# Optimization experiments

Hardware: AMD Instinct MI355X
Metric: run time of the kernel (lower is better)

## Reference

```python
import jax, jax.numpy as jnp
import numpy as np

# --- configuration (matches init_kwargs) ---
K = 8            # number of cluster fields
L = 8            # hashgrid levels
T = 2 ** 18      # hash table size per level (log2_hashmap_size=18)
F = 2            # features per level
HID = 64         # MLP hidden dim
BASE_RES = 16    # base resolution; max_res=2048 -> growth factor 2
N_PTS = 524288

PRIMES = np.array([1, 2654435761, 805459861], dtype=np.uint32)
RES = (BASE_RES * 2 ** np.arange(L)).astype(np.float32)  # [16,32,...,2048]
CORNERS = np.array([[i, j, k] for i in (0, 1) for j in (0, 1) for k in (0, 1)],
                   dtype=np.float32)  # [8,3] trilinear corner offsets


def setup_inputs() -> dict:
    key = jax.random.key(0)
    ks = jax.random.split(key, 6)
    return {
        "positions": jax.random.uniform(ks[0], (N_PTS, 3), dtype=jnp.float32),
        "centroids": jax.random.uniform(ks[1], (K, 3), dtype=jnp.float32),
        "tables":    jax.random.normal(ks[2], (K, L, T, F), dtype=jnp.float32) * 1e-2,
        "W1":        jax.random.normal(ks[3], (K, L * F, HID), dtype=jnp.float32) * 0.1,
        "b1":        jnp.zeros((K, HID), dtype=jnp.float32),
        "W2":        jax.random.normal(ks[4], (K, HID, 1), dtype=jnp.float32) * 0.1,
        "b2":        jnp.zeros((K, 1), dtype=jnp.float32),
    }


def _hash_encode(positions, tables, assign):
    """Multi-resolution hash encoding, table selected per-point by cluster assignment."""
    N = positions.shape[0]
    res = jnp.asarray(RES)                                    # [L]
    scaled = positions[:, None, :] * res[None, :, None]       # [N,L,3]
    f = jnp.floor(scaled)
    w = scaled - f                                            # [N,L,3] trilinear fracs
    corners = jnp.asarray(CORNERS)                            # [8,3]
    ci = (f[:, :, None, :] + corners[None, None]).astype(jnp.uint32)  # [N,L,8,3]
    p = jnp.asarray(PRIMES)
    h = (ci[..., 0] * p[0]) ^ (ci[..., 1] * p[1]) ^ (ci[..., 2] * p[2])
    h = (h & jnp.uint32(T - 1)).astype(jnp.int32)             # [N,L,8]
    lvl = jnp.arange(L, dtype=jnp.int32)
    # flat index into [K*L*T, F] table selects the assigned field's grid
    flat = (assign[:, None, None] * L + lvl[None, :, None]) * T + h   # [N,L,8]
    feats = tables.reshape(K * L * T, F)[flat]                # [N,L,8,F] gather
    cw = jnp.prod(jnp.where(corners[None, None] > 0.5,
                            w[:, :, None, :], 1.0 - w[:, :, None, :]), axis=-1)  # [N,L,8]
    enc = jnp.sum(feats * cw[..., None], axis=2)              # [N,L,F]
    return enc.reshape(N, L * F)


def reference(positions, centroids, tables, W1, b1, W2, b2):
    # cdist + argmin cluster routing
    d2 = jnp.sum((positions[:, None, :] - centroids[None]) ** 2, axis=-1)  # [N,K]
    assign = jnp.argmin(d2, axis=1).astype(jnp.int32)                      # [N]
    enc = _hash_encode(positions, tables, assign)                          # [N, L*F]
    dens = jnp.zeros((positions.shape[0], 1), dtype=positions.dtype)
    for k in range(K):  # small fixed loop over structurally distinct fields
        h = jax.nn.relu(enc @ W1[k] + b1[k])
        dk = jnp.exp(h @ W2[k] + b2[k])  # trunc_exp density activation
        dens = jnp.where((assign == k)[:, None], dk, dens)
    return dens  # [N,1]
```

## Files before the change

kernel.cpp:

```cpp
#include <hip/hip_runtime.h>
#include <hip/hip_fp16.h>
#include <math.h>

#define KF 8
#define LL 8
#define TT (1 << 18)
#define FF 2
#define HID 64
#define INF 16
#define W1S 1056
#define BS  68

#define NENT (KF * LL * TT)


__global__ __launch_bounds__(256) void repack_tables_fp16(
    const float4* __restrict__ src, uint4* __restrict__ dst, int nthreads)
{
    const int gid = blockIdx.x * blockDim.x + threadIdx.x;
    if (gid >= nthreads) return;
    const size_t b = (size_t)gid * 4;

    const float4 f0 = src[b + 0];
    const float4 f1 = src[b + 1];
    const float4 f2 = src[b + 2];
    const float4 f3 = src[b + 3];

    uint4 d0, d1;
    {
        __half2 h;
        h = __floats2half2_rn(f0.x, f0.y); d0.x = *reinterpret_cast<unsigned*>(&h);
        h = __floats2half2_rn(f0.z, f0.w); d0.y = *reinterpret_cast<unsigned*>(&h);
        h = __floats2half2_rn(f1.x, f1.y); d0.z = *reinterpret_cast<unsigned*>(&h);
        h = __floats2half2_rn(f1.z, f1.w); d0.w = *reinterpret_cast<unsigned*>(&h);
        h = __floats2half2_rn(f2.x, f2.y); d1.x = *reinterpret_cast<unsigned*>(&h);
        h = __floats2half2_rn(f2.z, f2.w); d1.y = *reinterpret_cast<unsigned*>(&h);
        h = __floats2half2_rn(f3.x, f3.y); d1.z = *reinterpret_cast<unsigned*>(&h);
        h = __floats2half2_rn(f3.z, f3.w); d1.w = *reinterpret_cast<unsigned*>(&h);
    }
    dst[(size_t)gid * 2 + 0] = d0;
    dst[(size_t)gid * 2 + 1] = d1;
}

__global__ __launch_bounds__(256) void propnet_density_kernel_h(
    const float* __restrict__ positions,
    const float* __restrict__ centroids,
    const __half2* __restrict__ tables,
    const float* __restrict__ W1,
    const float* __restrict__ b1,
    const float* __restrict__ W2,
    const float* __restrict__ b2,
    float* __restrict__ out,
    int npts)
{
    __shared__ float sW1[KF * W1S];
    __shared__ float sB1[KF * BS];
    __shared__ float sW2[KF * BS];
    __shared__ float sB2[KF];
    __shared__ float sC[KF * 3];

    const int tid = threadIdx.x;

    for (int idx = tid; idx < KF * INF * HID; idx += blockDim.x) {
        int k = idx >> 10;
        int r = idx & 1023;
        sW1[k * W1S + r] = W1[idx];
    }
    for (int idx = tid; idx < KF * HID; idx += blockDim.x) {
        int k = idx >> 6;
        int r = idx & 63;
        sB1[k * BS + r] = b1[idx];
        sW2[k * BS + r] = W2[idx];
    }
    if (tid < KF) sB2[tid] = b2[tid];
    if (tid < KF * 3) sC[tid] = centroids[tid];
    __syncthreads();

    const int gid = blockIdx.x * blockDim.x + tid;
    if (gid >= npts) return;

    const float px = positions[gid * 3 + 0];
    const float py = positions[gid * 3 + 1];
    const float pz = positions[gid * 3 + 2];

    int assign = 0;
    float best = 1e30f;
    #pragma unroll
    for (int k = 0; k < KF; ++k) {
        float dx = px - sC[k * 3 + 0];
        float dy = py - sC[k * 3 + 1];
        float dz = pz - sC[k * 3 + 2];
        float d2 = fmaf(dx, dx, fmaf(dy, dy, dz * dz));
        bool lt = d2 < best;
        assign = lt ? k : assign;
        best = lt ? d2 : best;
    }

    float enc[INF];
    const __half2* __restrict__ tab =
        tables + (size_t)assign * (LL * (size_t)TT);

    #pragma unroll
    for (int l = 0; l < LL; ++l) {
        const float res = (float)(16 << l);
        const float sx = px * res, sy = py * res, sz = pz * res;
        const float fx = floorf(sx), fy = floorf(sy), fz = floorf(sz);
        const float wx = sx - fx, wy = sy - fy, wz = sz - fz;
        const unsigned ix = (unsigned)(int)fx;
        const unsigned iy = (unsigned)(int)fy;
        const unsigned iz = (unsigned)(int)fz;

        const __half2* __restrict__ tl = tab + (size_t)l * TT;

        const unsigned hx0 = ix;
        const unsigned hx1 = ix + 1u;
        const unsigned hy0 = iy * 2654435761u;
        const unsigned hy1 = (iy + 1u) * 2654435761u;
        const unsigned hz0 = iz * 805459861u;
        const unsigned hz1 = (iz + 1u) * 805459861u;
        const unsigned M = TT - 1;

        const __half2 c000 = tl[(hx0 ^ hy0 ^ hz0) & M];
        const __half2 c001 = tl[(hx0 ^ hy0 ^ hz1) & M];
        const __half2 c010 = tl[(hx0 ^ hy1 ^ hz0) & M];
        const __half2 c011 = tl[(hx0 ^ hy1 ^ hz1) & M];
        const __half2 c100 = tl[(hx1 ^ hy0 ^ hz0) & M];
        const __half2 c101 = tl[(hx1 ^ hy0 ^ hz1) & M];
        const __half2 c110 = tl[(hx1 ^ hy1 ^ hz0) & M];
        const __half2 c111 = tl[(hx1 ^ hy1 ^ hz1) & M];

        const float ux = 1.f - wx, uy = 1.f - wy, uz = 1.f - wz;
        const float w000 = ux * uy * uz, w001 = ux * uy * wz;
        const float w010 = ux * wy * uz, w011 = ux * wy * wz;
        const float w100 = wx * uy * uz, w101 = wx * uy * wz;
        const float w110 = wx * wy * uz, w111 = wx * wy * wz;

        enc[l * 2 + 0] = __low2float(c000) * w000 + __low2float(c001) * w001
                       + __low2float(c010) * w010 + __low2float(c011) * w011
                       + __low2float(c100) * w100 + __low2float(c101) * w101
                       + __low2float(c110) * w110 + __low2float(c111) * w111;
        enc[l * 2 + 1] = __high2float(c000) * w000 + __high2float(c001) * w001
                       + __high2float(c010) * w010 + __high2float(c011) * w011
                       + __high2float(c100) * w100 + __high2float(c101) * w101
                       + __high2float(c110) * w110 + __high2float(c111) * w111;
    }

    const float4* __restrict__ w1k = (const float4*)(sW1 + assign * W1S);
    const float4* __restrict__ b1k = (const float4*)(sB1 + assign * BS);
    const float4* __restrict__ w2k = (const float4*)(sW2 + assign * BS);

    float outv = sB2[assign];
    #pragma unroll
    for (int j4 = 0; j4 < HID / 4; ++j4) {
        float4 a = b1k[j4];
        #pragma unroll
        for (int i = 0; i < INF; ++i) {
            const float4 w = w1k[i * (HID / 4) + j4];
            const float e = enc[i];
            a.x = fmaf(e, w.x, a.x);
            a.y = fmaf(e, w.y, a.y);
            a.z = fmaf(e, w.z, a.z);
            a.w = fmaf(e, w.w, a.w);
        }
        a.x = fmaxf(a.x, 0.f); a.y = fmaxf(a.y, 0.f);
        a.z = fmaxf(a.z, 0.f); a.w = fmaxf(a.w, 0.f);
        const float4 w2v = w2k[j4];
        outv = fmaf(a.x, w2v.x, outv);
        outv = fmaf(a.y, w2v.y, outv);
        outv = fmaf(a.z, w2v.z, outv);
        outv = fmaf(a.w, w2v.w, outv);
    }

    out[gid] = expf(outv);
}

__global__ __launch_bounds__(256) void propnet_density_kernel_f(
    const float* __restrict__ positions,
    const float* __restrict__ centroids,
    const float* __restrict__ tables,
    const float* __restrict__ W1,
    const float* __restrict__ b1,
    const float* __restrict__ W2,
    const float* __restrict__ b2,
    float* __restrict__ out,
    int npts)
{
    __shared__ float sW1[KF * W1S];
    __shared__ float sB1[KF * BS];
    __shared__ float sW2[KF * BS];
    __shared__ float sB2[KF];
    __shared__ float sC[KF * 3];

    const int tid = threadIdx.x;

    for (int idx = tid; idx < KF * INF * HID; idx += blockDim.x) {
        int k = idx >> 10;
        int r = idx & 1023;
        sW1[k * W1S + r] = W1[idx];
    }
    for (int idx = tid; idx < KF * HID; idx += blockDim.x) {
        int k = idx >> 6;
        int r = idx & 63;
        sB1[k * BS + r] = b1[idx];
        sW2[k * BS + r] = W2[idx];
    }
    if (tid < KF) sB2[tid] = b2[tid];
    if (tid < KF * 3) sC[tid] = centroids[tid];
    __syncthreads();

    const int gid = blockIdx.x * blockDim.x + tid;
    if (gid >= npts) return;

    const float px = positions[gid * 3 + 0];
    const float py = positions[gid * 3 + 1];
    const float pz = positions[gid * 3 + 2];

    int assign = 0;
    float best = 1e30f;
    #pragma unroll
    for (int k = 0; k < KF; ++k) {
        float dx = px - sC[k * 3 + 0];
        float dy = py - sC[k * 3 + 1];
        float dz = pz - sC[k * 3 + 2];
        float d2 = fmaf(dx, dx, fmaf(dy, dy, dz * dz));
        bool lt = d2 < best;
        assign = lt ? k : assign;
        best = lt ? d2 : best;
    }

    float enc[INF];
    const float2* __restrict__ tab =
        (const float2*)tables + (size_t)assign * (LL * (size_t)TT);

    #pragma unroll
    for (int l = 0; l < LL; ++l) {
        const float res = (float)(16 << l);
        const float sx = px * res, sy = py * res, sz = pz * res;
        const float fx = floorf(sx), fy = floorf(sy), fz = floorf(sz);
        const float wx = sx - fx, wy = sy - fy, wz = sz - fz;
        const unsigned ix = (unsigned)(int)fx;
        const unsigned iy = (unsigned)(int)fy;
        const unsigned iz = (unsigned)(int)fz;

        const float2* __restrict__ tl = tab + (size_t)l * TT;

        const unsigned hx0 = ix;
        const unsigned hx1 = ix + 1u;
        const unsigned hy0 = iy * 2654435761u;
        const unsigned hy1 = (iy + 1u) * 2654435761u;
        const unsigned hz0 = iz * 805459861u;
        const unsigned hz1 = (iz + 1u) * 805459861u;
        const unsigned M = TT - 1;

        const float2 c000 = tl[(hx0 ^ hy0 ^ hz0) & M];
        const float2 c001 = tl[(hx0 ^ hy0 ^ hz1) & M];
        const float2 c010 = tl[(hx0 ^ hy1 ^ hz0) & M];
        const float2 c011 = tl[(hx0 ^ hy1 ^ hz1) & M];
        const float2 c100 = tl[(hx1 ^ hy0 ^ hz0) & M];
        const float2 c101 = tl[(hx1 ^ hy0 ^ hz1) & M];
        const float2 c110 = tl[(hx1 ^ hy1 ^ hz0) & M];
        const float2 c111 = tl[(hx1 ^ hy1 ^ hz1) & M];

        const float ux = 1.f - wx, uy = 1.f - wy, uz = 1.f - wz;
        const float w000 = ux * uy * uz, w001 = ux * uy * wz;
        const float w010 = ux * wy * uz, w011 = ux * wy * wz;
        const float w100 = wx * uy * uz, w101 = wx * uy * wz;
        const float w110 = wx * wy * uz, w111 = wx * wy * wz;

        enc[l * 2 + 0] = c000.x * w000 + c001.x * w001 + c010.x * w010 + c011.x * w011
                       + c100.x * w100 + c101.x * w101 + c110.x * w110 + c111.x * w111;
        enc[l * 2 + 1] = c000.y * w000 + c001.y * w001 + c010.y * w010 + c011.y * w011
                       + c100.y * w100 + c101.y * w101 + c110.y * w110 + c111.y * w111;
    }

    const float4* __restrict__ w1k = (const float4*)(sW1 + assign * W1S);
    const float4* __restrict__ b1k = (const float4*)(sB1 + assign * BS);
    const float4* __restrict__ w2k = (const float4*)(sW2 + assign * BS);

    float outv = sB2[assign];
    #pragma unroll
    for (int j4 = 0; j4 < HID / 4; ++j4) {
        float4 a = b1k[j4];
        #pragma unroll
        for (int i = 0; i < INF; ++i) {
            const float4 w = w1k[i * (HID / 4) + j4];
            const float e = enc[i];
            a.x = fmaf(e, w.x, a.x);
            a.y = fmaf(e, w.y, a.y);
            a.z = fmaf(e, w.z, a.z);
            a.w = fmaf(e, w.w, a.w);
        }
        a.x = fmaxf(a.x, 0.f); a.y = fmaxf(a.y, 0.f);
        a.z = fmaxf(a.z, 0.f); a.w = fmaxf(a.w, 0.f);
        const float4 w2v = w2k[j4];
        outv = fmaf(a.x, w2v.x, outv);
        outv = fmaf(a.y, w2v.y, outv);
        outv = fmaf(a.z, w2v.z, outv);
        outv = fmaf(a.w, w2v.w, outv);
    }

    out[gid] = expf(outv);
}

extern "C" void kernel_launch(void* const* d_in, const int* in_sizes, int n_in,
                              void* d_out, int out_size, void* d_ws, size_t ws_size,
                              hipStream_t stream) {
    const float* positions = (const float*)d_in[0];
    const float* centroids = (const float*)d_in[1];
    const float* tables    = (const float*)d_in[2];
    const float* W1        = (const float*)d_in[3];
    const float* b1        = (const float*)d_in[4];
    const float* W2        = (const float*)d_in[5];
    const float* b2        = (const float*)d_in[6];
    float* out = (float*)d_out;

    const int npts = in_sizes[0] / 3;
    const int block = 256;
    const int grid = (npts + block - 1) / block;

    const size_t needed = (size_t)NENT * sizeof(__half2);
    if (ws_size >= needed && d_ws != nullptr) {
        const int nthreads = NENT / 8;
        const int rgrid = nthreads / 256;
        repack_tables_fp16<<<rgrid, 256, 0, stream>>>(
            (const float4*)tables, (uint4*)d_ws, nthreads);
        propnet_density_kernel_h<<<grid, block, 0, stream>>>(
            positions, centroids, (const __half2*)d_ws, W1, b1, W2, b2, out, npts);
    } else {
        propnet_density_kernel_f<<<grid, block, 0, stream>>>(
            positions, centroids, tables, W1, b1, W2, b2, out, npts);
    }
}
```

Baseline: 415.6 us.

## Bucket points by cluster before encoding so blocks run a single field

Adds a bucketing pass that computes each point's cluster assignment and scatters point indices into per-cluster lists using block-local and global atomic counters. The main kernel then launches 8x blocks, one cluster per block, so each block loads only that cluster's MLP weights into shared memory and all threads gather from one table. The aim is to cut shared-memory footprint (raising occupancy) and improve table locality. In exchange it adds two extra launches and an index buffer, makes position reads and output writes indirect (scattered), and launches many blocks that exit immediately.

Result: slower. 438.4 us (+5.5%).

```diff
diff --git a/kernel.cpp b/kernel.cpp
--- a/kernel.cpp
+++ b/kernel.cpp
@@ -12,6 +12,7 @@
 #define BS  68
 
 #define NENT (KF * LL * TT)
+#define TAB_BYTES ((size_t)NENT * 4)
 
 
 __global__ __launch_bounds__(256) void repack_tables_fp16(
@@ -42,63 +43,95 @@
     dst[(size_t)gid * 2 + 1] = d1;
 }
 
-__global__ __launch_bounds__(256) void propnet_density_kernel_h(
+__global__ void zero_cursors(unsigned* __restrict__ cursors)
+{
+    if (threadIdx.x < KF) cursors[threadIdx.x] = 0u;
+}
+
+__global__ __launch_bounds__(256) void bucket_points(
     const float* __restrict__ positions,
     const float* __restrict__ centroids,
+    unsigned* __restrict__ cursors,
+    unsigned* __restrict__ indices,
+    int npts)
+{
+    __shared__ float sC[KF * 3];
+    __shared__ unsigned lcnt[KF];
+    __shared__ unsigned lbase[KF];
+
+    const int tid = threadIdx.x;
+    if (tid < KF * 3) sC[tid] = centroids[tid];
+    if (tid < KF) lcnt[tid] = 0u;
+    __syncthreads();
+
+    const int gid = blockIdx.x * blockDim.x + tid;
+    int assign = 0;
+    unsigned lrank = 0;
+    const bool valid = (gid < npts);
+    if (valid) {
+        const float px = positions[gid * 3 + 0];
+        const float py = positions[gid * 3 + 1];
+        const float pz = positions[gid * 3 + 2];
+        float best = 1e30f;
+        #pragma unroll
+        for (int k = 0; k < KF; ++k) {
+            float dx = px - sC[k * 3 + 0];
+            float dy = py - sC[k * 3 + 1];
+            float dz = pz - sC[k * 3 + 2];
+            float d2 = fmaf(dx, dx, fmaf(dy, dy, dz * dz));
+            bool lt = d2 < best;
+            assign = lt ? k : assign;
+            best = lt ? d2 : best;
+        }
+        lrank = atomicAdd(&lcnt[assign], 1u);
+    }
+    __syncthreads();
+    if (tid < KF) lbase[tid] = atomicAdd(&cursors[tid], lcnt[tid]);
+    __syncthreads();
+    if (valid)
+        indices[(size_t)assign * npts + lbase[assign] + lrank] = (unsigned)gid;
+}
+
+__global__ __launch_bounds__(256) void propnet_density_bucketed(
+    const float* __restrict__ positions,
     const __half2* __restrict__ tables,
     const float* __restrict__ W1,
     const float* __restrict__ b1,
     const float* __restrict__ W2,
     const float* __restrict__ b2,
+    const unsigned* __restrict__ cursors,
+    const unsigned* __restrict__ indices,
     float* __restrict__ out,
     int npts)
 {
-    __shared__ float sW1[KF * W1S];
-    __shared__ float sB1[KF * BS];
-    __shared__ float sW2[KF * BS];
-    __shared__ float sB2[KF];
-    __shared__ float sC[KF * 3];
+    const int k = blockIdx.x & 7;
+    const int s = blockIdx.x >> 3;
+    const unsigned nk = cursors[k];
+    if ((unsigned)(s * 256) >= nk) return;
+
+    __shared__ float sW1[INF * HID];
+    __shared__ float sB1[HID];
+    __shared__ float sW2[HID];
 
     const int tid = threadIdx.x;
-
-    for (int idx = tid; idx < KF * INF * HID; idx += blockDim.x) {
-        int k = idx >> 10;
-        int r = idx & 1023;
-        sW1[k * W1S + r] = W1[idx];
-    }
-    for (int idx = tid; idx < KF * HID; idx += blockDim.x) {
-        int k = idx >> 6;
-        int r = idx & 63;
-        sB1[k * BS + r] = b1[idx];
-        sW2[k * BS + r] = W2[idx];
-    }
-    if (tid < KF) sB2[tid] = b2[tid];
-    if (tid < KF * 3) sC[tid] = centroids[tid];
+    for (int idx = tid; idx < INF * HID; idx += blockDim.x)
+        sW1[idx] = W1[k * (INF * HID) + idx];
+    if (tid < HID) {
+        sB1[tid] = b1[k * HID + tid];
+        sW2[tid] = W2[k * HID + tid];
+    }
     __syncthreads();
 
-    const int gid = blockIdx.x * blockDim.x + tid;
-    if (gid >= npts) return;
-
-    const float px = positions[gid * 3 + 0];
-    const float py = positions[gid * 3 + 1];
-    const float pz = positions[gid * 3 + 2];
-
-    int assign = 0;
-    float best = 1e30f;
-    #pragma unroll
-    for (int k = 0; k < KF; ++k) {
-        float dx = px - sC[k * 3 + 0];
-        float dy = py - sC[k * 3 + 1];
-        float dz = pz - sC[k * 3 + 2];
-        float d2 = fmaf(dx, dx, fmaf(dy, dy, dz * dz));
-        bool lt = d2 < best;
-        assign = lt ? k : assign;
-        best = lt ? d2 : best;
-    }
+    const unsigned pos_in_bucket = (unsigned)(s * 256 + tid);
+    if (pos_in_bucket >= nk) return;
+    const unsigned pidx = indices[(size_t)k * npts + pos_in_bucket];
+
+    const float px = positions[pidx * 3 + 0];
+    const float py = positions[pidx * 3 + 1];
+    const float pz = positions[pidx * 3 + 2];
 
     float enc[INF];
-    const __half2* __restrict__ tab =
-        tables + (size_t)assign * (LL * (size_t)TT);
+    const __half2* __restrict__ tab = tables + (size_t)k * (LL * (size_t)TT);
 
     #pragma unroll
     for (int l = 0; l < LL; ++l) {
@@ -145,11 +178,11 @@
                        + __high2float(c110) * w110 + __high2float(c111) * w111;
     }
 
-    const float4* __restrict__ w1k = (const float4*)(sW1 + assign * W1S);
-    const float4* __restrict__ b1k = (const float4*)(sB1 + assign * BS);
-    const float4* __restrict__ w2k = (const float4*)(sW2 + assign * BS);
-
-    float outv = sB2[assign];
+    const float4* __restrict__ w1k = (const float4*)sW1;
+    const float4* __restrict__ b1k = (const float4*)sB1;
+    const float4* __restrict__ w2k = (const float4*)sW2;
+
+    float outv = b2[k];
     #pragma unroll
     for (int j4 = 0; j4 < HID / 4; ++j4) {
         float4 a = b1k[j4];
@@ -171,13 +204,13 @@
         outv = fmaf(a.w, w2v.w, outv);
     }
 
-    out[gid] = expf(outv);
-}
-
-__global__ __launch_bounds__(256) void propnet_density_kernel_f(
+    out[pidx] = expf(outv);
+}
+
+__global__ __launch_bounds__(256) void propnet_density_kernel_h(
     const float* __restrict__ positions,
     const float* __restrict__ centroids,
-    const float* __restrict__ tables,
+    const __half2* __restrict__ tables,
     const float* __restrict__ W1,
     const float* __restrict__ b1,
     const float* __restrict__ W2,
@@ -229,8 +262,8 @@
     }
 
     float enc[INF];
-    const float2* __restrict__ tab =
-        (const float2*)tables + (size_t)assign * (LL * (size_t)TT);
+    const __half2* __restrict__ tab =
+        tables + (size_t)assign * (LL * (size_t)TT);
 
     #pragma unroll
     for (int l = 0; l < LL; ++l) {
@@ -242,7 +275,7 @@
         const unsigned iy = (unsigned)(int)fy;
         const unsigned iz = (unsigned)(int)fz;
 
-        const float2* __restrict__ tl = tab + (size_t)l * TT;
+        const __half2* __restrict__ tl = tab + (size_t)l * TT;
 
         const unsigned hx0 = ix;
         const unsigned hx1 = ix + 1u;
@@ -252,14 +285,14 @@
         const unsigned hz1 = (iz + 1u) * 805459861u;
         const unsigned M = TT - 1;
 
-        const float2 c000 = tl[(hx0 ^ hy0 ^ hz0) & M];
-        const float2 c001 = tl[(hx0 ^ hy0 ^ hz1) & M];
-        const float2 c010 = tl[(hx0 ^ hy1 ^ hz0) & M];
-        const float2 c011 = tl[(hx0 ^ hy1 ^ hz1) & M];
-        const float2 c100 = tl[(hx1 ^ hy0 ^ hz0) & M];
-        const float2 c101 = tl[(hx1 ^ hy0 ^ hz1) & M];
-        const float2 c110 = tl[(hx1 ^ hy1 ^ hz0) & M];
-        const float2 c111 = tl[(hx1 ^ hy1 ^ hz1) & M];
+        const __half2 c000 = tl[(hx0 ^ hy0 ^ hz0) & M];
+        const __half2 c001 = tl[(hx0 ^ hy0 ^ hz1) & M];
+        const __half2 c010 = tl[(hx0 ^ hy1 ^ hz0) & M];
+        const __half2 c011 = tl[(hx0 ^ hy1 ^ hz1) & M];
+        const __half2 c100 = tl[(hx1 ^ hy0 ^ hz0) & M];
+        const __half2 c101 = tl[(hx1 ^ hy0 ^ hz1) & M];
+        const __half2 c110 = tl[(hx1 ^ hy1 ^ hz0) & M];
+        const __half2 c111 = tl[(hx1 ^ hy1 ^ hz1) & M];
 
         const float ux = 1.f - wx, uy = 1.f - wy, uz = 1.f - wz;
         const float w000 = ux * uy * uz, w001 = ux * uy * wz;
@@ -267,10 +300,14 @@
         const float w100 = wx * uy * uz, w101 = wx * uy * wz;
         const float w110 = wx * wy * uz, w111 = wx * wy * wz;
 
-        enc[l * 2 + 0] = c000.x * w000 + c001.x * w001 + c010.x * w010 + c011.x * w011
-                       + c100.x * w100 + c101.x * w101 + c110.x * w110 + c111.x * w111;
-        enc[l * 2 + 1] = c000.y * w000 + c001.y * w001 + c010.y * w010 + c011.y * w011
-                       + c100.y * w100 + c101.y * w101 + c110.y * w110 + c111.y * w111;
+        enc[l * 2 + 0] = __low2float(c000) * w000 + __low2float(c001) * w001
+                       + __low2float(c010) * w010 + __low2float(c011) * w011
+                       + __low2float(c100) * w100 + __low2float(c101) * w101
+                       + __low2float(c110) * w110 + __low2float(c111) * w111;
+        enc[l * 2 + 1] = __high2float(c000) * w000 + __high2float(c001) * w001
+                       + __high2float(c010) * w010 + __high2float(c011) * w011
+                       + __high2float(c100) * w100 + __high2float(c101) * w101
+                       + __high2float(c110) * w110 + __high2float(c111) * w111;
     }
 
     const float4* __restrict__ w1k = (const float4*)(sW1 + assign * W1S);
@@ -302,6 +339,134 @@
     out[gid] = expf(outv);
 }
 
+__global__ __launch_bounds__(256) void propnet_density_kernel_f(
+    const float* __restrict__ positions,
+    const float* __restrict__ centroids,
+    const float* __restrict__ tables,
+    const float* __restrict__ W1,
+    const float* __restrict__ b1,
+    const float* __restrict__ W2,
+    const float* __restrict__ b2,
+    float* __restrict__ out,
+    int npts)
+{
+    __shared__ float sW1[KF * W1S];
+    __shared__ float sB1[KF * BS];
+    __shared__ float sW2[KF * BS];
+    __shared__ float sB2[KF];
+    __shared__ float sC[KF * 3];
+
+    const int tid = threadIdx.x;
+
+    for (int idx = tid; idx < KF * INF * HID; idx += blockDim.x) {
+        int k = idx >> 10;
+        int r = idx & 1023;
+        sW1[k * W1S + r] = W1[idx];
+    }
+    for (int idx = tid; idx < KF * HID; idx += blockDim.x) {
+        int k = idx >> 6;
+        int r = idx & 63;
+        sB1[k * BS + r] = b1[idx];
+        sW2[k * BS + r] = W2[idx];
+    }
+    if (tid < KF) sB2[tid] = b2[tid];
+    if (tid < KF * 3) sC[tid] = centroids[tid];
+    __syncthreads();
+
+    const int gid = blockIdx.x * blockDim.x + tid;
+    if (gid >= npts) return;
+
+    const float px = positions[gid * 3 + 0];
+    const float py = positions[gid * 3 + 1];
+    const float pz = positions[gid * 3 + 2];
+
+    int assign = 0;
+    float best = 1e30f;
+    #pragma unroll
+    for (int k = 0; k < KF; ++k) {
+        float dx = px - sC[k * 3 + 0];
+        float dy = py - sC[k * 3 + 1];
+        float dz = pz - sC[k * 3 + 2];
+        float d2 = fmaf(dx, dx, fmaf(dy, dy, dz * dz));
+        bool lt = d2 < best;
+        assign = lt ? k : assign;
+        best = lt ? d2 : best;
+    }
+
+    float enc[INF];
+    const float2* __restrict__ tab =
+        (const float2*)tables + (size_t)assign * (LL * (size_t)TT);
+
+    #pragma unroll
+    for (int l = 0; l < LL; ++l) {
+        const float res = (float)(16 << l);
+        const float sx = px * res, sy = py * res, sz = pz * res;
+        const float fx = floorf(sx), fy = floorf(sy), fz = floorf(sz);
+        const float wx = sx - fx, wy = sy - fy, wz = sz - fz;
+        const unsigned ix = (unsigned)(int)fx;
+        const unsigned iy = (unsigned)(int)fy;
+        const unsigned iz = (unsigned)(int)fz;
+
+        const float2* __restrict__ tl = tab + (size_t)l * TT;
+
+        const unsigned hx0 = ix;
+        const unsigned hx1 = ix + 1u;
+        const unsigned hy0 = iy * 2654435761u;
+        const unsigned hy1 = (iy + 1u) * 2654435761u;
+        const unsigned hz0 = iz * 805459861u;
+        const unsigned hz1 = (iz + 1u) * 805459861u;
+        const unsigned M = TT - 1;
+
+        const float2 c000 = tl[(hx0 ^ hy0 ^ hz0) & M];
+        const float2 c001 = tl[(hx0 ^ hy0 ^ hz1) & M];
+        const float2 c010 = tl[(hx0 ^ hy1 ^ hz0) & M];
+        const float2 c011 = tl[(hx0 ^ hy1 ^ hz1) & M];
+        const float2 c100 = tl[(hx1 ^ hy0 ^ hz0) & M];
+        const float2 c101 = tl[(hx1 ^ hy0 ^ hz1) & M];
+        const float2 c110 = tl[(hx1 ^ hy1 ^ hz0) & M];
+        const float2 c111 = tl[(hx1 ^ hy1 ^ hz1) & M];
+
+        const float ux = 1.f - wx, uy = 1.f - wy, uz = 1.f - wz;
+        const float w000 = ux * uy * uz, w001 = ux * uy * wz;
+        const float w010 = ux * wy * uz, w011 = ux * wy * wz;
+        const float w100 = wx * uy * uz, w101 = wx * uy * wz;
+        const float w110 = wx * wy * uz, w111 = wx * wy * wz;
+
+        enc[l * 2 + 0] = c000.x * w000 + c001.x * w001 + c010.x * w010 + c011.x * w011
+                       + c100.x * w100 + c101.x * w101 + c110.x * w110 + c111.x * w111;
+        enc[l * 2 + 1] = c000.y * w000 + c001.y * w001 + c010.y * w010 + c011.y * w011
+                       + c100.y * w100 + c101.y * w101 + c110.y * w110 + c111.y * w111;
+    }
+
+    const float4* __restrict__ w1k = (const float4*)(sW1 + assign * W1S);
+    const float4* __restrict__ b1k = (const float4*)(sB1 + assign * BS);
+    const float4* __restrict__ w2k = (const float4*)(sW2 + assign * BS);
+
+    float outv = sB2[assign];
+    #pragma unroll
+    for (int j4 = 0; j4 < HID / 4; ++j4) {
+        float4 a = b1k[j4];
+        #pragma unroll
+        for (int i = 0; i < INF; ++i) {
+            const float4 w = w1k[i * (HID / 4) + j4];
+            const float e = enc[i];
+            a.x = fmaf(e, w.x, a.x);
+            a.y = fmaf(e, w.y, a.y);
+            a.z = fmaf(e, w.z, a.z);
+            a.w = fmaf(e, w.w, a.w);
+        }
+        a.x = fmaxf(a.x, 0.f); a.y = fmaxf(a.y, 0.f);
+        a.z = fmaxf(a.z, 0.f); a.w = fmaxf(a.w, 0.f);
+        const float4 w2v = w2k[j4];
+        outv = fmaf(a.x, w2v.x, outv);
+        outv = fmaf(a.y, w2v.y, outv);
+        outv = fmaf(a.z, w2v.z, outv);
+        outv = fmaf(a.w, w2v.w, outv);
+    }
+
+    out[gid] = expf(outv);
+}
+
 extern "C" void kernel_launch(void* const* d_in, const int* in_sizes, int n_in,
                               void* d_out, int out_size, void* d_ws, size_t ws_size,
                               hipStream_t stream) {
@@ -316,18 +481,33 @@
 
     const int npts = in_sizes[0] / 3;
     const int block = 256;
-    const int grid = (npts + block - 1) / block;
-
-    const size_t needed = (size_t)NENT * sizeof(__half2);
-    if (ws_size >= needed && d_ws != nullptr) {
-        const int nthreads = NENT / 8;
-        const int rgrid = nthreads / 256;
-        repack_tables_fp16<<<rgrid, 256, 0, stream>>>(
-            (const float4*)tables, (uint4*)d_ws, nthreads);
-        propnet_density_kernel_h<<<grid, block, 0, stream>>>(
+    const int nb = (npts + block - 1) / block;
+
+    const size_t need_h    = TAB_BYTES;
+    const size_t need_full = TAB_BYTES + 256 + (size_t)KF * npts * 4;
+
+    if (ws_size >= need_full && d_ws != nullptr) {
+        char* base = (char*)d_ws;
+        __half2*  wsTab   = (__half2*)base;
+        unsigned* cursors = (unsigned*)(base + TAB_BYTES);
+        unsigned* indices = (unsigned*)(base + TAB_BYTES + 256);
+
+        const int rthreads = NENT / 8;
+        repack_tables_fp16<<<rthreads / 256, 256, 0, stream>>>(
+            (const float4*)tables, (uint4*)wsTab, rthreads);
+        zero_cursors<<<1, 64, 0, stream>>>(cursors);
+        bucket_points<<<nb, block, 0, stream>>>(
+            positions, centroids, cursors, indices, npts);
+        propnet_density_bucketed<<<8 * nb, block, 0, stream>>>(
+            positions, wsTab, W1, b1, W2, b2, cursors, indices, out, npts);
+    } else if (ws_size >= need_h && d_ws != nullptr) {
+        const int rthreads = NENT / 8;
+        repack_tables_fp16<<<rthreads / 256, 256, 0, stream>>>(
+            (const float4*)tables, (uint4*)d_ws, rthreads);
+        propnet_density_kernel_h<<<nb, block, 0, stream>>>(
             positions, centroids, (const __half2*)d_ws, W1, b1, W2, b2, out, npts);
     } else {
-        propnet_density_kernel_f<<<grid, block, 0, stream>>>(
+        propnet_density_kernel_f<<<nb, block, 0, stream>>>(
             positions, centroids, tables, W1, b1, W2, b2, out, npts);
     }
 }
```
